# Kernel optimization log

Measured on AMD Instinct MI355X. Metric: run time of the kernel, lower is better.

## Reference

```python
import jax, jax.numpy as jnp
import numpy as np

N = 50000      # nodes
E = 800000     # edges (before self-loops)
G = 64         # graphs in batch
IN, HID, OUT, H = 128, 64, 64, 4
NEG_SLOPE = 0.2
BN_EPS = 1e-5


def setup_inputs() -> dict:
    key = jax.random.key(0)
    ks = jax.random.split(key, 16)
    s = 0.1
    return {
        "x": jax.random.normal(ks[0], (N, IN), jnp.float32),
        "edge_index": jax.random.randint(ks[1], (2, E), 0, N, dtype=jnp.int64),
        "batch": jnp.sort(jax.random.randint(ks[2], (N,), 0, G, dtype=jnp.int64)),
        "num_graphs": G,
        "W1": jax.random.normal(ks[3], (IN, H * HID), jnp.float32) * s,
        "att_src1": jax.random.normal(ks[4], (H, HID), jnp.float32) * s,
        "att_dst1": jax.random.normal(ks[5], (H, HID), jnp.float32) * s,
        "b1": jnp.zeros((HID,), jnp.float32),
        "W2": jax.random.normal(ks[6], (HID, H * OUT), jnp.float32) * s,
        "att_src2": jax.random.normal(ks[7], (H, OUT), jnp.float32) * s,
        "att_dst2": jax.random.normal(ks[8], (H, OUT), jnp.float32) * s,
        "b2": jnp.zeros((OUT,), jnp.float32),
        "gate_w1": jax.random.normal(ks[9], (OUT, OUT), jnp.float32) * s,
        "gate_b1": jnp.zeros((OUT,), jnp.float32),
        "bn_gamma": jnp.ones((OUT,), jnp.float32),
        "bn_beta": jnp.zeros((OUT,), jnp.float32),
        "gate_w2": jax.random.normal(ks[10], (OUT, 1), jnp.float32) * s,
        "gate_b2": jnp.zeros((1,), jnp.float32),
        "lin_w": jax.random.normal(ks[11], (OUT, 1), jnp.float32) * s,
        "lin_b": jnp.zeros((1,), jnp.float32),
    }


def segment_softmax(e, seg, num_segments):
    # numerically stable softmax over segments (per-destination / per-graph)
    m = jax.ops.segment_max(e, seg, num_segments=num_segments)
    m = jnp.where(jnp.isfinite(m), m, 0.0)
    ex = jnp.exp(e - m[seg])
    den = jax.ops.segment_sum(ex, seg, num_segments=num_segments)
    return ex / (den[seg] + 1e-16)


def gat_conv(x, src, dst, n, W, a_src, a_dst, b, heads, ch):
    h = (x @ W).reshape(n, heads, ch)                 # [N,H,C]
    asrc = jnp.sum(h * a_src, axis=-1)                # [N,H]
    adst = jnp.sum(h * a_dst, axis=-1)                # [N,H]
    e = jax.nn.leaky_relu(asrc[src] + adst[dst], NEG_SLOPE)   # [E',H]
    alpha = segment_softmax(e, dst, n)                # softmax over incoming edges
    out = jax.ops.segment_sum(h[src] * alpha[:, :, None], dst, num_segments=n)
    return jnp.mean(out, axis=1) + b                  # concat=False -> head mean


def reference(x, edge_index, batch, num_graphs, W1, att_src1, att_dst1, b1,
              W2, att_src2, att_dst2, b2, gate_w1, gate_b1, bn_gamma, bn_beta,
              gate_w2, gate_b2, lin_w, lin_b):
    n = x.shape[0]
    loop = jnp.arange(n, dtype=edge_index.dtype)      # PyG add_self_loops default
    src = jnp.concatenate([edge_index[0], loop])
    dst = jnp.concatenate([edge_index[1], loop])

    out = jax.nn.sigmoid(gat_conv(x, src, dst, n, W1, att_src1, att_dst1, b1, H, HID))
    out = jax.nn.sigmoid(gat_conv(out, src, dst, n, W2, att_src2, att_dst2, b2, H, OUT))

    # GlobalAttention pooling; gate_nn = Linear -> BN(eval, rm=0, rv=1) -> ReLU -> Linear
    g = out @ gate_w1 + gate_b1
    g = (g / jnp.sqrt(1.0 + BN_EPS)) * bn_gamma + bn_beta
    g = jax.nn.relu(g) @ gate_w2 + gate_b2            # [N,1]
    gate = segment_softmax(g, batch, num_graphs)      # per-graph softmax
    pooled = jax.ops.segment_sum(gate * out, batch, num_segments=num_graphs)  # [G,OUT]

    return jax.nn.sigmoid(pooled @ lin_w + lin_b)     # [G,1]
```

## Files before the change

### kernel.cpp

```cpp
#include <hip/hip_runtime.h>


constexpr int NN = 50000;
constexpr int EE = 800000;
constexpr int E2 = EE + NN;
constexpr int NG = 64;
constexpr float NEG = 0.2f;
constexpr int MT = NN / 16;
constexpr int SLOTS = 64;
constexpr int CH = 16;
constexpr int GB = (MT + 3) / 4;
constexpr int EDGE_NB = (E2 + 255) / 256;
constexpr int ZERO_NB = (NN + 255) / 256;

using bf16x8 = __attribute__((ext_vector_type(8))) __bf16;
using f32x4  = __attribute__((ext_vector_type(4))) float;
using f32x2  = __attribute__((ext_vector_type(2))) float;

__device__ __forceinline__ float wred(float v) {
#pragma unroll
  for (int o = 32; o; o >>= 1) v += __shfl_down(v, o);
  return v;
}
__device__ __forceinline__ float sigmoidf(float v) { return 1.f / (1.f + __expf(-v)); }
__device__ __forceinline__ float lrelu(float v) { return fmaxf(v, NEG * v); }
__device__ __forceinline__ unsigned short f2b(float f) {
  union { float f; unsigned u; } v; v.f = f;
  unsigned r = v.u + 0x7fff + ((v.u >> 16) & 1);
  return (unsigned short)(r >> 16);
}
__device__ __forceinline__ float b2f(unsigned short b) {
  union { unsigned u; float f; } v; v.u = ((unsigned)b) << 16;
  return v.f;
}

__global__ void prep_kernel(const float* __restrict__ W1, const float* __restrict__ W2,
                            const float* __restrict__ gw1, const float* __restrict__ gamma,
                            const int* __restrict__ batch, int* __restrict__ cnt,
                            unsigned short* __restrict__ W1b, unsigned short* __restrict__ W2b,
                            unsigned short* __restrict__ Bg, int* __restrict__ goffs) {
  int b = blockIdx.x;
  if (b < ZERO_NB) {
    int i = b * 256 + threadIdx.x;
    if (i < NN) cnt[i] = 0;
    return;
  }
  if (b < ZERO_NB + 128) {
    int idx = (b - ZERO_NB) * 256 + threadIdx.x;
    int j = idx & 7, lane = (idx >> 3) & 63, rest = idx >> 9;
    int kc = rest & 3, ntile = rest >> 2;
    W1b[idx] = f2b(W1[(kc * 32 + (lane >> 4) * 8 + j) * 256 + ntile * 16 + (lane & 15)]);
    return;
  }
  if (b < ZERO_NB + 192) {
    int idx = (b - ZERO_NB - 128) * 256 + threadIdx.x;
    int j = idx & 7, lane = (idx >> 3) & 63, rest = idx >> 9;
    int kc = rest & 1, ntile = rest >> 1;
    W2b[idx] = f2b(W2[(kc * 32 + (lane >> 4) * 8 + j) * 256 + ntile * 16 + (lane & 15)]);
    return;
  }
  if (b < ZERO_NB + 208) {
    int idx = (b - ZERO_NB - 192) * 256 + threadIdx.x;
    int j = idx & 7, lane = (idx >> 3) & 63, rest = idx >> 9;
    int kc = rest & 1, nt = rest >> 1;
    int k = kc * 32 + (lane >> 4) * 8 + j;
    int n = nt * 16 + (lane & 15);
    Bg[idx] = f2b(gw1[k * 64 + n] * gamma[n] * rsqrtf(1.f + 1e-5f));
    return;
  }
  int g = threadIdx.x;
  if (g <= NG) {
    int lo = 0, hi = NN;
    while (lo < hi) {
      int mid = (lo + hi) >> 1;
      if (batch[mid] < g) lo = mid + 1; else hi = mid;
    }
    goffs[g] = lo;
  }
}

template <int K, bool A32>
__device__ __forceinline__ void gemm_body(int mt, int lane,
                                          const void* __restrict__ A_raw,
                                          const unsigned short* __restrict__ Bp,
                                          unsigned char* __restrict__ C8,
                                          const float* __restrict__ att_s,
                                          const float* __restrict__ att_d,
                                          float* __restrict__ asrc,
                                          float* __restrict__ adst) {
  constexpr int KC = K / 32;
  int m0 = mt * 16;
  int q = lane >> 4, r = lane & 15;
  f32x4 acc[16] = {};
#pragma unroll
  for (int kc = 0; kc < KC; ++kc) {
    bf16x8 a;
    if constexpr (A32) {
      const float* Arow = (const float*)A_raw + (size_t)(m0 + r) * K + q * 8 + kc * 32;
      float4 f0 = *(const float4*)Arow;
      float4 f1 = *(const float4*)(Arow + 4);
      union { bf16x8 v; unsigned short s[8]; } u;
      u.s[0] = f2b(f0.x); u.s[1] = f2b(f0.y); u.s[2] = f2b(f0.z); u.s[3] = f2b(f0.w);
      u.s[4] = f2b(f1.x); u.s[5] = f2b(f1.y); u.s[6] = f2b(f1.z); u.s[7] = f2b(f1.w);
      a = u.v;
    } else {
      a = *(const bf16x8*)((const unsigned short*)A_raw +
                           (size_t)(m0 + r) * K + q * 8 + kc * 32);
    }
#pragma unroll
    for (int nt = 0; nt < 16; ++nt) {
      bf16x8 b = *(const bf16x8*)&Bp[(((size_t)nt * KC + kc) * 64 + lane) * 8];
      acc[nt] = __builtin_amdgcn_mfma_f32_16x16x32_bf16(a, b, acc[nt], 0, 0, 0);
    }
  }
#pragma unroll
  for (int nt = 0; nt < 16; ++nt) {
    unsigned col = nt * 16 + r;
#pragma unroll
    for (int reg = 0; reg < 4; ++reg) {
      unsigned row = m0 + q * 4 + reg;
      int p = __builtin_amdgcn_cvt_pk_fp8_f32(acc[nt][reg], 0.f, 0, false);
      C8[row * 256u + col] = (unsigned char)(p & 0xff);
    }
  }
  float ps[4][4] = {}, pd[4][4] = {};
#pragma unroll
  for (int head = 0; head < 4; ++head) {
#pragma unroll
    for (int i = 0; i < 4; ++i) {
      float sv = att_s[head * 64 + i * 16 + r];
      float dv = att_d[head * 64 + i * 16 + r];
#pragma unroll
      for (int reg = 0; reg < 4; ++reg) {
        ps[head][reg] += acc[head * 4 + i][reg] * sv;
        pd[head][reg] += acc[head * 4 + i][reg] * dv;
      }
    }
  }
#pragma unroll
  for (int head = 0; head < 4; ++head)
#pragma unroll
    for (int reg = 0; reg < 4; ++reg)
#pragma unroll
      for (int o = 1; o < 16; o <<= 1) {
        ps[head][reg] += __shfl_xor(ps[head][reg], o);
        pd[head][reg] += __shfl_xor(pd[head][reg], o);
      }
  if (r == 0) {
#pragma unroll
    for (int reg = 0; reg < 4; ++reg) {
      int row = m0 + q * 4 + reg;
#pragma unroll
      for (int head = 0; head < 4; ++head) {
        asrc[row * 4 + head] = ps[head][reg];
        adst[row * 4 + head] = pd[head][reg];
      }
    }
  }
}

__global__ void gemm1_build_kernel(const float* __restrict__ x,
                                   const unsigned short* __restrict__ W1b,
                                   unsigned char* __restrict__ C8,
                                   const float* __restrict__ att_s,
                                   const float* __restrict__ att_d,
                                   float* __restrict__ asrc, float* __restrict__ adst,
                                   const int* __restrict__ ei, int* __restrict__ cnt,
                                   int* __restrict__ csr_src) {
  int b = blockIdx.x;
  if (b < GB) {
    int wave = threadIdx.x >> 6, lane = threadIdx.x & 63;
    int mt = b * 4 + wave;
    if (mt >= MT) return;
    gemm_body<128, true>(mt, lane, x, W1b, C8, att_s, att_d, asrc, adst);
    return;
  }
  int e = (b - GB) * 256 + threadIdx.x;
  if (e >= E2) return;
  int src, dst;
  if (e < EE) { src = ei[e]; dst = ei[EE + e]; }
  else { src = dst = e - EE; }
  int rank = atomicAdd(&cnt[dst], 1);
  if (rank < SLOTS) csr_src[(unsigned)dst * SLOTS + rank] = src;
}

__global__ void gemm2_kernel(const unsigned short* __restrict__ out1b,
                             const unsigned short* __restrict__ W2b,
                             unsigned char* __restrict__ C8,
                             const float* __restrict__ att_s,
                             const float* __restrict__ att_d,
                             float* __restrict__ asrc, float* __restrict__ adst) {
  int wave = threadIdx.x >> 6, lane = threadIdx.x & 63;
  int mt = blockIdx.x * 4 + wave;
  if (mt >= MT) return;
  gemm_body<64, false>(mt, lane, out1b, W2b, C8, att_s, att_d, asrc, adst);
}

__global__ void aggregate_kernel(const unsigned char* __restrict__ h8,
                                 const float* __restrict__ asrc,
                                 const float* __restrict__ adst,
                                 const int* __restrict__ cnt,
                                 const int* __restrict__ csr_src,
                                 const float* __restrict__ bias,
                                 unsigned short* __restrict__ outb) {
  int wave = threadIdx.x >> 6, lane = threadIdx.x & 63;
  int node = blockIdx.x * 4 + wave;
  if (node >= NN) return;
  int deg = min(cnt[node], SLOTS);
  int hgrp = lane >> 4;
  int hb = lane & 48;
  float adh = adst[node * 4 + hgrp];
  int src_all = csr_src[(unsigned)node * SLOTS + lane];
  float wreg[4];
  float den = 0.f;
#pragma unroll
  for (int i = 0; i < 4; ++i) {
    int slot = i * 16 + (lane & 15);
    int s = __shfl(src_all, slot);
    bool valid = slot < deg;
    float xv = asrc[(unsigned)(valid ? s : 0) * 4 + hgrp];
    float w = __expf(lrelu(xv + adh));
    wreg[i] = valid ? w : 0.f;
    den += wreg[i];
  }
#pragma unroll
  for (int o = 1; o < 16; o <<= 1) den += __shfl_xor(den, o);
  const unsigned char* hp = h8 + (unsigned)lane * 4;
  f32x2 a01 = {0.f, 0.f}, a23 = {0.f, 0.f};
  int e = 0;
#pragma unroll
  for (int i = 0; i < 4; ++i) {
    if (e >= deg) break;
    float wcur = wreg[i];
    int bound = min(deg, (i + 1) * 16);
    for (; e + 3 < bound; e += 4) {
      int s0 = __shfl(src_all, e),     s1 = __shfl(src_all, e + 1);
      int s2 = __shfl(src_all, e + 2), s3 = __shfl(src_all, e + 3);
      float w0 = __shfl(wcur, ((e)     & 15) | hb);
      float w1 = __shfl(wcur, ((e + 1) & 15) | hb);
      float w2 = __shfl(wcur, ((e + 2) & 15) | hb);
      float w3 = __shfl(wcur, ((e + 3) & 15) | hb);
      unsigned d0 = *(const unsigned*)(hp + ((unsigned)s0 << 8));
      unsigned d1 = *(const unsigned*)(hp + ((unsigned)s1 << 8));
      unsigned d2 = *(const unsigned*)(hp + ((unsigned)s2 << 8));
      unsigned d3 = *(const unsigned*)(hp + ((unsigned)s3 << 8));
      f32x2 l0 = __builtin_amdgcn_cvt_pk_f32_fp8(d0, false), u0 = __builtin_amdgcn_cvt_pk_f32_fp8(d0, true);
      f32x2 l1 = __builtin_amdgcn_cvt_pk_f32_fp8(d1, false), u1 = __builtin_amdgcn_cvt_pk_f32_fp8(d1, true);
      f32x2 l2 = __builtin_amdgcn_cvt_pk_f32_fp8(d2, false), u2 = __builtin_amdgcn_cvt_pk_f32_fp8(d2, true);
      f32x2 l3 = __builtin_amdgcn_cvt_pk_f32_fp8(d3, false), u3 = __builtin_amdgcn_cvt_pk_f32_fp8(d3, true);
      a01 += l0 * w0; a23 += u0 * w0;
      a01 += l1 * w1; a23 += u1 * w1;
      a01 += l2 * w2; a23 += u2 * w2;
      a01 += l3 * w3; a23 += u3 * w3;
    }
    for (; e < bound; ++e) {
      int s0 = __shfl(src_all, e);
      float w0 = __shfl(wcur, (e & 15) | hb);
      unsigned d0 = *(const unsigned*)(hp + ((unsigned)s0 << 8));
      f32x2 l0 = __builtin_amdgcn_cvt_pk_f32_fp8(d0, false), u0 = __builtin_amdgcn_cvt_pk_f32_fp8(d0, true);
      a01 += l0 * w0; a23 += u0 * w0;
    }
  }
  float inv = 1.f / (den + 1e-16f);
  float r0 = a01.x * inv, r1 = a01.y * inv, r2 = a23.x * inv, r3 = a23.y * inv;
  r0 += __shfl_xor(r0, 16); r0 += __shfl_xor(r0, 32);
  r1 += __shfl_xor(r1, 16); r1 += __shfl_xor(r1, 32);
  r2 += __shfl_xor(r2, 16); r2 += __shfl_xor(r2, 32);
  r3 += __shfl_xor(r3, 16); r3 += __shfl_xor(r3, 32);
  if (lane < 16) {
    float4 bv = *(const float4*)&bias[lane * 4];
    ushort4 o;
    o.x = f2b(sigmoidf(0.25f * r0 + bv.x));
    o.y = f2b(sigmoidf(0.25f * r1 + bv.y));
    o.z = f2b(sigmoidf(0.25f * r2 + bv.z));
    o.w = f2b(sigmoidf(0.25f * r3 + bv.w));
    *(ushort4*)&outb[(size_t)node * 64 + lane * 4] = o;
  }
}

__global__ void pool_partial_kernel(const int* __restrict__ goffs,
                                    const unsigned short* __restrict__ out2b,
                                    const unsigned short* __restrict__ Bg,
                                    const float* __restrict__ gb1,
                                    const float* __restrict__ gamma,
                                    const float* __restrict__ beta,
                                    const float* __restrict__ gw2,
                                    const float* __restrict__ gb2,
                                    float* __restrict__ part_acc,
                                    float* __restrict__ part_den) {
  int b = blockIdx.x, j = blockIdx.y;
  int beg = goffs[b], end = goffs[b + 1];
  int chunk = (end - beg + CH - 1) / CH;
  int cb = beg + j * chunk;
  int ce = min(end, cb + chunk);
  int lane = threadIdx.x & 63, wave = threadIdx.x >> 6;
  int q = lane >> 4, r = lane & 15;
  const float s = rsqrtf(1.f + 1e-5f);
  float gb2v = gb2[0];
  float accv = 0.f, den = 0.f;
  for (int n0 = cb + wave * 16; n0 < ce; n0 += 64) {
    f32x4 acc[4] = {};
    int row = n0 + r;
    if (row >= NN) row = NN - 1;
    const unsigned short* Arow = out2b + (size_t)row * 64 + q * 8;
#pragma unroll
    for (int kc = 0; kc < 2; ++kc) {
      bf16x8 a = *(const bf16x8*)(Arow + kc * 32);
#pragma unroll
      for (int nt = 0; nt < 4; ++nt) {
        bf16x8 b8 = *(const bf16x8*)&Bg[(((size_t)nt * 2 + kc) * 64 + lane) * 8];
        acc[nt] = __builtin_amdgcn_mfma_f32_16x16x32_bf16(a, b8, acc[nt], 0, 0, 0);
      }
    }
    float sum[4] = {0.f, 0.f, 0.f, 0.f};
#pragma unroll
    for (int nt = 0; nt < 4; ++nt) {
      int col = nt * 16 + r;
      float off = gb1[col] * gamma[col] * s + beta[col];
      float w2 = gw2[col];
#pragma unroll
      for (int reg = 0; reg < 4; ++reg)
        sum[reg] += fmaxf(acc[nt][reg] + off, 0.f) * w2;
    }
#pragma unroll
    for (int reg = 0; reg < 4; ++reg)
#pragma unroll
      for (int o = 1; o < 16; o <<= 1) sum[reg] += __shfl_xor(sum[reg], o);
    float gx[4];
#pragma unroll
    for (int reg = 0; reg < 4; ++reg) {
      int n = n0 + q * 4 + reg;
      gx[reg] = (n < ce) ? __expf(sum[reg] + gb2v) : 0.f;
    }
#pragma unroll
    for (int t = 0; t < 16; ++t) {
      int n = n0 + t;
      if (n >= ce) break;
      float gv = __shfl(gx[t & 3], (t >> 2) << 4);
      accv += gv * b2f(out2b[(size_t)n * 64 + lane]);
      den += gv;
    }
  }
  __shared__ float sacc[4][64];
  __shared__ float sden[4];
  sacc[wave][lane] = accv;
  if (lane == 0) sden[wave] = den;
  __syncthreads();
  if (wave == 0) {
    float a = sacc[0][lane] + sacc[1][lane] + sacc[2][lane] + sacc[3][lane];
    part_acc[((size_t)b * CH + j) * 64 + lane] = a;
    if (lane == 0) part_den[b * CH + j] = sden[0] + sden[1] + sden[2] + sden[3];
  }
}

__global__ void pool_final_kernel(const float* __restrict__ part_acc,
                                  const float* __restrict__ part_den,
                                  const float* __restrict__ lw, const float* __restrict__ lb,
                                  float* __restrict__ out) {
  int b = blockIdx.x, lane = threadIdx.x;
  float a = 0.f;
#pragma unroll
  for (int j = 0; j < CH; ++j) a += part_acc[((size_t)b * CH + j) * 64 + lane];
  float den = (lane < CH) ? part_den[b * CH + lane] : 0.f;
  den = wred(den);
  den = __shfl(den, 0);
  float p = a / (den + 1e-16f);
  float v = wred(p * lw[lane]);
  if (lane == 0) out[b] = sigmoidf(v + lb[0]);
}

extern "C" void kernel_launch(void* const* d_in, const int* in_sizes, int n_in,
                              void* d_out, int out_size, void* d_ws, size_t ws_size,
                              hipStream_t stream) {
  const float* x    = (const float*)d_in[0];
  const int*   ei   = (const int*)d_in[1];
  const int*   batch= (const int*)d_in[2];
  const float* W1   = (const float*)d_in[4];
  const float* as1  = (const float*)d_in[5];
  const float* ad1  = (const float*)d_in[6];
  const float* b1   = (const float*)d_in[7];
  const float* W2   = (const float*)d_in[8];
  const float* as2  = (const float*)d_in[9];
  const float* ad2  = (const float*)d_in[10];
  const float* b2   = (const float*)d_in[11];
  const float* gw1  = (const float*)d_in[12];
  const float* gb1  = (const float*)d_in[13];
  const float* gamma= (const float*)d_in[14];
  const float* beta = (const float*)d_in[15];
  const float* gw2  = (const float*)d_in[16];
  const float* gb2  = (const float*)d_in[17];
  const float* lw   = (const float*)d_in[18];
  const float* lb   = (const float*)d_in[19];
  float* out = (float*)d_out;

  char* ws = (char*)d_ws;
  size_t off = 0;
  auto alloc = [&](size_t bytes) -> void* {
    void* p = ws + off;
    off = (off + bytes + 255) & ~(size_t)255;
    return p;
  };
  unsigned short* W1b    = (unsigned short*)alloc((size_t)128 * 256 * 2);
  unsigned short* W2b    = (unsigned short*)alloc((size_t)64 * 256 * 2);
  unsigned short* Bg     = (unsigned short*)alloc((size_t)64 * 64 * 2);
  unsigned char*  h8     = (unsigned char*)alloc((size_t)NN * 256);
  unsigned short* out1b  = (unsigned short*)alloc((size_t)NN * 64 * 2);
  unsigned short* out2b  = (unsigned short*)alloc((size_t)NN * 64 * 2);
  float*    asrc    = (float*)alloc((size_t)NN * 4 * 4);
  float*    adst    = (float*)alloc((size_t)NN * 4 * 4);
  int*      cnt     = (int*)alloc((size_t)NN * 4);
  int*      csr_src = (int*)alloc((size_t)NN * SLOTS * 4);
  int*      goffs   = (int*)alloc((size_t)(NG + 1) * 4);
  float*    pacc    = (float*)alloc((size_t)NG * CH * 64 * 4);
  float*    pden    = (float*)alloc((size_t)NG * CH * 4);

  const int nodeBlocks = (NN + 3) / 4;

  prep_kernel<<<ZERO_NB + 209, 256, 0, stream>>>(W1, W2, gw1, gamma, batch, cnt,
                                                 W1b, W2b, Bg, goffs);

  gemm1_build_kernel<<<GB + EDGE_NB, 256, 0, stream>>>(x, W1b, h8, as1, ad1, asrc, adst,
                                                       ei, cnt, csr_src);
  aggregate_kernel<<<nodeBlocks, 256, 0, stream>>>(h8, asrc, adst, cnt, csr_src, b1, out1b);

  gemm2_kernel<<<GB, 256, 0, stream>>>(out1b, W2b, h8, as2, ad2, asrc, adst);
  aggregate_kernel<<<nodeBlocks, 256, 0, stream>>>(h8, asrc, adst, cnt, csr_src, b2, out2b);

  pool_partial_kernel<<<dim3(NG, CH), 256, 0, stream>>>(goffs, out2b, Bg, gb1, gamma, beta,
                                                        gw2, gb2, pacc, pden);
  pool_final_kernel<<<NG, 64, 0, stream>>>(pacc, pden, lw, lb, out);
}
```

Measured before the change: 265.0 us.

## Build CSR via two-pass bucketed binning with 16-bit source indices

Result: faster. 257.1 us (-3.0%).

```diff
diff --git a/kernel.cpp b/kernel.cpp
--- a/kernel.cpp
+++ b/kernel.cpp
@@ -3,15 +3,18 @@
 
 constexpr int NN = 50000;
 constexpr int EE = 800000;
-constexpr int E2 = EE + NN;
 constexpr int NG = 64;
 constexpr float NEG = 0.2f;
 constexpr int MT = NN / 16;
 constexpr int SLOTS = 64;
 constexpr int CH = 16;
 constexpr int GB = (MT + 3) / 4;
-constexpr int EDGE_NB = (E2 + 255) / 256;
-constexpr int ZERO_NB = (NN + 255) / 256;
+
+constexpr int EB_EDGES = 4096;
+constexpr int EBN = (EE + EB_EDGES - 1) / EB_EDGES;
+constexpr int NBKT = (NN + 255) / 256;
+constexpr int CAP = 48;
+constexpr int OVFCAP = 8192;
 
 using bf16x8 = __attribute__((ext_vector_type(8))) __bf16;
 using f32x4  = __attribute__((ext_vector_type(4))) float;
@@ -36,31 +39,27 @@
 
 __global__ void prep_kernel(const float* __restrict__ W1, const float* __restrict__ W2,
                             const float* __restrict__ gw1, const float* __restrict__ gamma,
-                            const int* __restrict__ batch, int* __restrict__ cnt,
+                            const int* __restrict__ batch,
                             unsigned short* __restrict__ W1b, unsigned short* __restrict__ W2b,
-                            unsigned short* __restrict__ Bg, int* __restrict__ goffs) {
+                            unsigned short* __restrict__ Bg, int* __restrict__ goffs,
+                            int* __restrict__ ovf_cnt) {
   int b = blockIdx.x;
-  if (b < ZERO_NB) {
-    int i = b * 256 + threadIdx.x;
-    if (i < NN) cnt[i] = 0;
-    return;
-  }
-  if (b < ZERO_NB + 128) {
-    int idx = (b - ZERO_NB) * 256 + threadIdx.x;
+  if (b < 128) {
+    int idx = b * 256 + threadIdx.x;
     int j = idx & 7, lane = (idx >> 3) & 63, rest = idx >> 9;
     int kc = rest & 3, ntile = rest >> 2;
     W1b[idx] = f2b(W1[(kc * 32 + (lane >> 4) * 8 + j) * 256 + ntile * 16 + (lane & 15)]);
     return;
   }
-  if (b < ZERO_NB + 192) {
-    int idx = (b - ZERO_NB - 128) * 256 + threadIdx.x;
+  if (b < 192) {
+    int idx = (b - 128) * 256 + threadIdx.x;
     int j = idx & 7, lane = (idx >> 3) & 63, rest = idx >> 9;
     int kc = rest & 1, ntile = rest >> 1;
     W2b[idx] = f2b(W2[(kc * 32 + (lane >> 4) * 8 + j) * 256 + ntile * 16 + (lane & 15)]);
     return;
   }
-  if (b < ZERO_NB + 208) {
-    int idx = (b - ZERO_NB - 192) * 256 + threadIdx.x;
+  if (b < 208) {
+    int idx = (b - 192) * 256 + threadIdx.x;
     int j = idx & 7, lane = (idx >> 3) & 63, rest = idx >> 9;
     int kc = rest & 1, nt = rest >> 1;
     int k = kc * 32 + (lane >> 4) * 8 + j;
@@ -68,6 +67,7 @@
     Bg[idx] = f2b(gw1[k * 64 + n] * gamma[n] * rsqrtf(1.f + 1e-5f));
     return;
   }
+  if (threadIdx.x == 0) *ovf_cnt = 0;
   int g = threadIdx.x;
   if (g <= NG) {
     int lo = 0, hi = NN;
@@ -165,8 +165,11 @@
                                    const float* __restrict__ att_s,
                                    const float* __restrict__ att_d,
                                    float* __restrict__ asrc, float* __restrict__ adst,
-                                   const int* __restrict__ ei, int* __restrict__ cnt,
-                                   int* __restrict__ csr_src) {
+                                   const int* __restrict__ ei,
+                                   unsigned* __restrict__ bins,
+                                   int* __restrict__ binCnt,
+                                   int* __restrict__ ovf_cnt,
+                                   unsigned* __restrict__ ovf) {
   int b = blockIdx.x;
   if (b < GB) {
     int wave = threadIdx.x >> 6, lane = threadIdx.x & 63;
@@ -175,32 +178,89 @@
     gemm_body<128, true>(mt, lane, x, W1b, C8, att_s, att_d, asrc, adst);
     return;
   }
-  int e = (b - GB) * 256 + threadIdx.x;
-  if (e >= E2) return;
-  int src, dst;
-  if (e < EE) { src = ei[e]; dst = ei[EE + e]; }
-  else { src = dst = e - EE; }
-  int rank = atomicAdd(&cnt[dst], 1);
-  if (rank < SLOTS) csr_src[(unsigned)dst * SLOTS + rank] = src;
-}
-
-__global__ void gemm2_kernel(const unsigned short* __restrict__ out1b,
-                             const unsigned short* __restrict__ W2b,
-                             unsigned char* __restrict__ C8,
-                             const float* __restrict__ att_s,
-                             const float* __restrict__ att_d,
-                             float* __restrict__ asrc, float* __restrict__ adst) {
-  int wave = threadIdx.x >> 6, lane = threadIdx.x & 63;
-  int mt = blockIdx.x * 4 + wave;
-  if (mt >= MT) return;
-  gemm_body<64, false>(mt, lane, out1b, W2b, C8, att_s, att_d, asrc, adst);
+  int hb = b - GB;
+  __shared__ int hist[NBKT];
+  for (int t = threadIdx.x; t < NBKT; t += 256) hist[t] = 0;
+  __syncthreads();
+  int e0 = hb * EB_EDGES + threadIdx.x * 16;
+#pragma unroll
+  for (int k4 = 0; k4 < 4; ++k4) {
+    int e = e0 + k4 * 4;
+    if (e >= EE) break;
+    int4 s4 = *(const int4*)&ei[e];
+    int4 d4 = *(const int4*)&ei[EE + e];
+    int ss[4] = {s4.x, s4.y, s4.z, s4.w};
+    int dd[4] = {d4.x, d4.y, d4.z, d4.w};
+#pragma unroll
+    for (int u = 0; u < 4; ++u) {
+      if (e + u >= EE) break;
+      int src = ss[u], dst = dd[u];
+      int bkt = dst >> 8;
+      int r = atomicAdd(&hist[bkt], 1);
+      if (r < CAP) {
+        bins[((unsigned)hb * NBKT + bkt) * CAP + r] =
+            (unsigned)src | ((unsigned)(dst & 255) << 16);
+      } else {
+        int o = atomicAdd(ovf_cnt, 1);
+        if (o < OVFCAP) ovf[o] = (unsigned)src | ((unsigned)dst << 16);
+      }
+    }
+  }
+  __syncthreads();
+  for (int t = threadIdx.x; t < NBKT; t += 256) binCnt[hb * NBKT + t] = hist[t];
+}
+
+__global__ __launch_bounds__(1024) void csr_build_kernel(
+    const unsigned* __restrict__ bins, const int* __restrict__ binCnt,
+    const int* __restrict__ ovf_cnt, const unsigned* __restrict__ ovf,
+    unsigned short* __restrict__ csr16, int* __restrict__ cnt) {
+  int b = blockIdx.x;
+  __shared__ int hist[256];
+  int t = threadIdx.x;
+  int node0 = b << 8;
+  if (t < 256) {
+    hist[t] = 1;
+    int node = node0 + t;
+    if (node < NN) csr16[(unsigned)node * SLOTS] = (unsigned short)node;
+  }
+  __syncthreads();
+  int wave = t >> 6, lane = t & 63;
+  for (int i = wave; i < EBN; i += 16) {
+    int c = binCnt[i * NBKT + b];
+    if (c > CAP) c = CAP;
+    for (int base = 0; base < c; base += 64) {
+      int j = base + lane;
+      if (j < c) {
+        unsigned p = bins[((unsigned)i * NBKT + b) * CAP + j];
+        int dl = p >> 16, src = p & 0xffff;
+        int r = atomicAdd(&hist[dl], 1);
+        if (r < SLOTS) csr16[(unsigned)(node0 + dl) * SLOTS + r] = (unsigned short)src;
+      }
+    }
+  }
+  __syncthreads();
+  int oc = *ovf_cnt;
+  if (oc > OVFCAP) oc = OVFCAP;
+  for (int j = t; j < oc; j += 1024) {
+    unsigned p = ovf[j];
+    int dst = (int)(p >> 16);
+    if ((dst >> 8) == b) {
+      int r = atomicAdd(&hist[dst & 255], 1);
+      if (r < SLOTS) csr16[(unsigned)dst * SLOTS + r] = (unsigned short)(p & 0xffff);
+    }
+  }
+  __syncthreads();
+  if (t < 256) {
+    int node = node0 + t;
+    if (node < NN) cnt[node] = hist[t];
+  }
 }
 
 __global__ void aggregate_kernel(const unsigned char* __restrict__ h8,
                                  const float* __restrict__ asrc,
                                  const float* __restrict__ adst,
                                  const int* __restrict__ cnt,
-                                 const int* __restrict__ csr_src,
+                                 const unsigned short* __restrict__ csr_src,
                                  const float* __restrict__ bias,
                                  unsigned short* __restrict__ outb) {
   int wave = threadIdx.x >> 6, lane = threadIdx.x & 63;
@@ -276,6 +336,18 @@
     o.w = f2b(sigmoidf(0.25f * r3 + bv.w));
     *(ushort4*)&outb[(size_t)node * 64 + lane * 4] = o;
   }
+}
+
+__global__ void gemm2_kernel(const unsigned short* __restrict__ out1b,
+                             const unsigned short* __restrict__ W2b,
+                             unsigned char* __restrict__ C8,
+                             const float* __restrict__ att_s,
+                             const float* __restrict__ att_d,
+                             float* __restrict__ asrc, float* __restrict__ adst) {
+  int wave = threadIdx.x >> 6, lane = threadIdx.x & 63;
+  int mt = blockIdx.x * 4 + wave;
+  if (mt >= MT) return;
+  gemm_body<64, false>(mt, lane, out1b, W2b, C8, att_s, att_d, asrc, adst);
 }
 
 __global__ void pool_partial_kernel(const int* __restrict__ goffs,
@@ -409,22 +481,28 @@
   float*    asrc    = (float*)alloc((size_t)NN * 4 * 4);
   float*    adst    = (float*)alloc((size_t)NN * 4 * 4);
   int*      cnt     = (int*)alloc((size_t)NN * 4);
-  int*      csr_src = (int*)alloc((size_t)NN * SLOTS * 4);
+  unsigned short* csr16 = (unsigned short*)alloc((size_t)NN * SLOTS * 2);
+  unsigned* bins    = (unsigned*)alloc((size_t)EBN * NBKT * CAP * 4);
+  int*      binCnt  = (int*)alloc((size_t)EBN * NBKT * 4);
+  int*      ovf_cnt = (int*)alloc(256);
+  unsigned* ovf     = (unsigned*)alloc((size_t)OVFCAP * 4);
   int*      goffs   = (int*)alloc((size_t)(NG + 1) * 4);
   float*    pacc    = (float*)alloc((size_t)NG * CH * 64 * 4);
   float*    pden    = (float*)alloc((size_t)NG * CH * 4);
 
   const int nodeBlocks = (NN + 3) / 4;
 
-  prep_kernel<<<ZERO_NB + 209, 256, 0, stream>>>(W1, W2, gw1, gamma, batch, cnt,
-                                                 W1b, W2b, Bg, goffs);
-
-  gemm1_build_kernel<<<GB + EDGE_NB, 256, 0, stream>>>(x, W1b, h8, as1, ad1, asrc, adst,
-                                                       ei, cnt, csr_src);
-  aggregate_kernel<<<nodeBlocks, 256, 0, stream>>>(h8, asrc, adst, cnt, csr_src, b1, out1b);
+  prep_kernel<<<209, 256, 0, stream>>>(W1, W2, gw1, gamma, batch,
+                                       W1b, W2b, Bg, goffs, ovf_cnt);
+
+  gemm1_build_kernel<<<GB + EBN, 256, 0, stream>>>(x, W1b, h8, as1, ad1, asrc, adst,
+                                                   ei, bins, binCnt, ovf_cnt, ovf);
+  csr_build_kernel<<<NBKT, 1024, 0, stream>>>(bins, binCnt, ovf_cnt, ovf, csr16, cnt);
+
+  aggregate_kernel<<<nodeBlocks, 256, 0, stream>>>(h8, asrc, adst, cnt, csr16, b1, out1b);
 
   gemm2_kernel<<<GB, 256, 0, stream>>>(out1b, W2b, h8, as2, ad2, asrc, adst);
-  aggregate_kernel<<<nodeBlocks, 256, 0, stream>>>(h8, asrc, adst, cnt, csr_src, b2, out2b);
+  aggregate_kernel<<<nodeBlocks, 256, 0, stream>>>(h8, asrc, adst, cnt, csr16, b2, out2b);
 
   pool_partial_kernel<<<dim3(NG, CH), 256, 0, stream>>>(goffs, out2b, Bg, gb1, gamma, beta,
                                                         gw2, gb2, pacc, pden);
```
